# Performance work log

Measured on AMD Instinct MI355X. Metric: run time of the kernel, lower is better.

Reference implementation:

```python
import jax, jax.numpy as jnp
import numpy as np

N_EDGES = 1048576
N_CENTERS = 32768
N_SPECIES = 4
L_MAX = 3
N_BASIS = 12
N_MAX = 8
R_CUT = 5.0
NORM = 1.0 / np.sqrt(32.0)  # hypers['normalize'] = avg_num_neighbors = 32
SH_SPLITS = [0, 1, 4, 9, 16]  # cumulative offsets of (2l+1)


def real_sph_harm_lmax3(u):
    # u: [E,3] unit vectors; returns [E,16] real normalized spherical harmonics (sphericart order m=-l..l)
    x, y, z = u[:, 0], u[:, 1], u[:, 2]
    c0 = 0.5 * np.sqrt(1.0 / np.pi)
    c1 = np.sqrt(3.0 / (4.0 * np.pi))
    x2, y2, z2 = x * x, y * y, z * z
    sh = [
        jnp.full_like(x, c0),
        c1 * y, c1 * z, c1 * x,
        0.5 * np.sqrt(15.0 / np.pi) * x * y,
        0.5 * np.sqrt(15.0 / np.pi) * y * z,
        0.25 * np.sqrt(5.0 / np.pi) * (3.0 * z2 - 1.0),
        0.5 * np.sqrt(15.0 / np.pi) * x * z,
        0.25 * np.sqrt(15.0 / np.pi) * (x2 - y2),
        0.25 * np.sqrt(35.0 / (2.0 * np.pi)) * y * (3.0 * x2 - y2),
        0.5 * np.sqrt(105.0 / np.pi) * x * y * z,
        0.25 * np.sqrt(21.0 / (2.0 * np.pi)) * y * (5.0 * z2 - 1.0),
        0.25 * np.sqrt(7.0 / np.pi) * (5.0 * z2 * z - 3.0 * z),
        0.25 * np.sqrt(21.0 / (2.0 * np.pi)) * x * (5.0 * z2 - 1.0),
        0.25 * np.sqrt(105.0 / np.pi) * z * (x2 - y2),
        0.25 * np.sqrt(35.0 / (2.0 * np.pi)) * x * (x2 - y2),
    ]
    return jnp.stack(sh, axis=1)


def setup_inputs() -> dict:
    key = jax.random.key(0)
    k1, k2, k3, k4 = jax.random.split(key, 4)
    vectors = jax.random.normal(k1, (N_EDGES, 3), dtype=jnp.float32) * 1.5
    radial_weights = jax.random.normal(k2, (L_MAX + 1, N_BASIS, N_MAX), dtype=jnp.float32) * 0.1
    center_index = jax.random.randint(k3, (N_EDGES,), 0, N_CENTERS, dtype=jnp.int64)
    neighbor_species_index = jax.random.randint(k4, (N_EDGES,), 0, N_SPECIES, dtype=jnp.int64)
    return {"vectors": vectors, "radial_weights": radial_weights,
            "center_index": center_index, "neighbor_species_index": neighbor_species_index}


def reference(vectors, radial_weights, center_index, neighbor_species_index):
    # distances and unit vectors
    r = jnp.sqrt(jnp.sum(vectors * vectors, axis=-1) + 1e-12)  # [E]
    u = vectors / r[:, None]
    # smooth radial basis phi_n(r) = sin((n+1) pi r / r_cut)/r, normalized (LE-like)
    ns = jnp.arange(1, N_BASIS + 1, dtype=vectors.dtype)
    phi = jnp.sin(np.pi / R_CUT * r[:, None] * ns[None, :]) / r[:, None] * NORM  # [E, N_BASIS]
    sh = real_sph_harm_lmax3(u)  # [E,16]
    # scatter target: (center, neighbor_species) channel
    idx = center_index * N_SPECIES + neighbor_species_index  # [E]
    densities = []
    for l in range(L_MAX + 1):
        m_l = 2 * l + 1
        sh_l = jax.lax.slice_in_dim(sh, SH_SPLITS[l], SH_SPLITS[l + 1], axis=1)  # [E, 2l+1]
        rad_l = phi @ radial_weights[l]  # [E, N_MAX]
        edge_l = rad_l[:, None, :] * sh_l[:, :, None]  # [E, 2l+1, N_MAX] outer product
        dens = jax.ops.segment_sum(edge_l.reshape(edge_l.shape[0], -1), idx,
                                   num_segments=N_CENTERS * N_SPECIES)  # [N*S, m*n]
        dens = dens.reshape(N_CENTERS, N_SPECIES, m_l, N_MAX)
        dens = jnp.transpose(dens, (0, 2, 1, 3)).reshape(N_CENTERS, m_l, N_SPECIES * N_MAX)
        densities.append(dens)  # c^{a_i l}_{Ai, m, a_j n}
    # concatenate the per-l TensorMap blocks along the m axis -> [N, sum(2l+1), S*N_MAX]
    return jnp.concatenate(densities, axis=1)
```

## Files before the change

kernel.cpp:

```cpp
#include <hip/hip_runtime.h>
#include <math.h>

#define N_EDGES     1048576
#define NBKT        4096
#define SEG_PER_BKT 32
#define N_BASIS     12
#define CAP         384
#define HBLK        64
#define HEPB        (N_EDGES / HBLK)

#define WS_BLKHIST  0
#define WS_TOTALS   (HBLK * NBKT * 2)
#define WS_OFFSETS  (WS_TOTALS + NBKT * 4)
#define WS_REC      (WS_OFFSETS + NBKT * 4)
#define WS_NEED     (WS_REC + (size_t)N_EDGES * 16)

__device__ __forceinline__ void compute_edge(float x, float y, float z,
                                             float* __restrict__ ph,
                                             float* __restrict__ sh)
{
    const float r2    = fmaf(x, x, fmaf(y, y, z * z)) + 1e-12f;
    const float inv_r = rsqrtf(r2);
    const float r     = r2 * inv_r;
    x *= inv_r; y *= inv_r; z *= inv_r;

    const float t = 0.6283185307179586f * r;
    float s1, c1;
    __sincosf(t, &s1, &c1);
    const float twoc = 2.0f * c1;
    const float scale = 0.17677669529663687f * inv_r;
    float skm1 = 0.0f, sk = s1;
    #pragma unroll
    for (int b = 0; b < N_BASIS; ++b) {
        ph[b] = sk * scale;
        const float nxt = fmaf(twoc, sk, -skm1);
        skm1 = sk; sk = nxt;
    }

    const float x2 = x * x, y2 = y * y, z2 = z * z;
    sh[0]  = 0.28209479177387814f;
    sh[1]  = 0.4886025119029199f * y;
    sh[2]  = 0.4886025119029199f * z;
    sh[3]  = 0.4886025119029199f * x;
    sh[4]  = 1.0925484305920792f * x * y;
    sh[5]  = 1.0925484305920792f * y * z;
    sh[6]  = 0.31539156525252005f * (3.0f * z2 - 1.0f);
    sh[7]  = 1.0925484305920792f * x * z;
    sh[8]  = 0.5462742152960396f * (x2 - y2);
    sh[9]  = 0.5900435899266435f * y * (3.0f * x2 - y2);
    sh[10] = 2.890611442640554f  * x * y * z;
    sh[11] = 0.4570457994644658f * y * (5.0f * z2 - 1.0f);
    sh[12] = 0.3731763325901154f * (5.0f * z2 * z - 3.0f * z);
    sh[13] = 0.4570457994644658f * x * (5.0f * z2 - 1.0f);
    sh[14] = 1.445305721320277f  * z * (x2 - y2);
    sh[15] = 0.5900435899266435f * x * (x2 - y2);
}

__global__ __launch_bounds__(1024) void hist_kernel(
    const int* __restrict__ cidx, const int* __restrict__ sidx,
    unsigned short* __restrict__ blkhist)
{
    __shared__ int h[NBKT];
    const int t = threadIdx.x;
    #pragma unroll
    for (int i = t; i < NBKT; i += 1024) h[i] = 0;
    __syncthreads();
    const int base = blockIdx.x * HEPB;
    #pragma unroll
    for (int k = 0; k < HEPB / 1024; ++k) {
        const int e = base + k * 1024 + t;
        const int seg = (cidx[e] << 2) | sidx[e];
        atomicAdd(&h[seg >> 5], 1);
    }
    __syncthreads();
    #pragma unroll
    for (int i = t; i < NBKT; i += 1024)
        blkhist[blockIdx.x * NBKT + i] = (unsigned short)h[i];
}

__global__ __launch_bounds__(1024) void partition16_kernel(
    const int* __restrict__ cidx, const int* __restrict__ sidx,
    const float* __restrict__ vectors,
    const unsigned short* __restrict__ blkhist,
    float4* __restrict__ rec16,
    int* __restrict__ offsets_g, int* __restrict__ totals_g)
{
    __shared__ int ps[1024];
    __shared__ int bb[NBKT];
    __shared__ int lcnt[NBKT];
    const int t  = threadIdx.x;
    const int me = blockIdx.x;

    int tot0 = 0, tot1 = 0, tot2 = 0, tot3 = 0;
    int bef0 = 0, bef1 = 0, bef2 = 0, bef3 = 0;
    for (int blk = 0; blk < HBLK; ++blk) {
        const ushort4 hv = ((const ushort4*)(blkhist + blk * NBKT))[t];
        tot0 += hv.x; tot1 += hv.y; tot2 += hv.z; tot3 += hv.w;
        if (blk < me) { bef0 += hv.x; bef1 += hv.y; bef2 += hv.z; bef3 += hv.w; }
    }
    const int quad = tot0 + tot1 + tot2 + tot3;
    ps[t] = quad;
    __syncthreads();
    #pragma unroll
    for (int d = 1; d < 1024; d <<= 1) {
        const int v = (t >= d) ? ps[t - d] : 0;
        __syncthreads();
        ps[t] += v;
        __syncthreads();
    }
    const int ex = ps[t] - quad;
    const int e0 = ex, e1 = ex + tot0, e2 = e1 + tot1, e3 = e2 + tot2;
    bb[4 * t + 0] = e0 + bef0;
    bb[4 * t + 1] = e1 + bef1;
    bb[4 * t + 2] = e2 + bef2;
    bb[4 * t + 3] = e3 + bef3;
    lcnt[4 * t + 0] = 0; lcnt[4 * t + 1] = 0;
    lcnt[4 * t + 2] = 0; lcnt[4 * t + 3] = 0;
    if (me == 0) {
        offsets_g[4 * t + 0] = e0;  totals_g[4 * t + 0] = tot0;
        offsets_g[4 * t + 1] = e1;  totals_g[4 * t + 1] = tot1;
        offsets_g[4 * t + 2] = e2;  totals_g[4 * t + 2] = tot2;
        offsets_g[4 * t + 3] = e3;  totals_g[4 * t + 3] = tot3;
    }
    __syncthreads();

    const int base = me * HEPB;
    #pragma unroll
    for (int k = 0; k < HEPB / 1024; ++k) {
        const int e = base + k * 1024 + t;
        const int seg = (cidx[e] << 2) | sidx[e];
        const int bkt = seg >> 5;
        const float x = vectors[3 * e + 0];
        const float y = vectors[3 * e + 1];
        const float z = vectors[3 * e + 2];
        const int r = atomicAdd(&lcnt[bkt], 1);
        rec16[bb[bkt] + r] = make_float4(x, y, z, __int_as_float(seg & 31));
    }
}

__global__ __launch_bounds__(256) void compute16_kernel(
    const float4* __restrict__ rec16,
    const int* __restrict__ offsets, const int* __restrict__ counts,
    const float* __restrict__ rw,
    float* __restrict__ out)
{
    __shared__ float4 pay[CAP * 7];
    __shared__ int shist[SEG_PER_BKT];
    __shared__ int soff[SEG_PER_BKT + 1];
    __shared__ int scur[SEG_PER_BKT];

    const int t = threadIdx.x;
    const int b = blockIdx.x;
    const int n = t & 7;
    const int g = t >> 3;

    const int off = offsets[b];
    const int cnt = counts[b];

    if (cnt > CAP) {
        float Wn[4][N_BASIS];
        #pragma unroll
        for (int l = 0; l < 4; ++l)
            #pragma unroll
            for (int bb2 = 0; bb2 < N_BASIS; ++bb2)
                Wn[l][bb2] = rw[(l * N_BASIS + bb2) * 8 + n];
        float acc[16];
        #pragma unroll
        for (int L = 0; L < 16; ++L) acc[L] = 0.0f;
        for (int j = 0; j < cnt; ++j) {
            const float4 v = rec16[off + j];
            if (__float_as_int(v.w) != g) continue;
            float ph[N_BASIS], sh[16];
            compute_edge(v.x, v.y, v.z, ph, sh);
            float rad[4];
            #pragma unroll
            for (int l = 0; l < 4; ++l) {
                float a = 0.0f;
                #pragma unroll
                for (int bb2 = 0; bb2 < N_BASIS; ++bb2)
                    a = fmaf(ph[bb2], Wn[l][bb2], a);
                rad[l] = a;
            }
            #pragma unroll
            for (int L = 0; L < 16; ++L) {
                const int l = (L == 0) ? 0 : (L < 4) ? 1 : (L < 9) ? 2 : 3;
                acc[L] = fmaf(sh[L], rad[l], acc[L]);
            }
        }
        const int seg = b * SEG_PER_BKT + g;
        float* op = out + (size_t)(seg >> 2) * 512 + (seg & 3) * 8 + n;
        #pragma unroll
        for (int L = 0; L < 16; ++L) op[L * 32] = acc[L];
        return;
    }

    if (t < SEG_PER_BKT) shist[t] = 0;
    __syncthreads();

    float4 recs[2];
    const int iters = (cnt + 255) >> 8;
    #pragma unroll
    for (int it = 0; it < 2; ++it) {
        const int i = it * 256 + t;
        if (it < iters && i < cnt) {
            recs[it] = rec16[off + i];
            atomicAdd(&shist[__float_as_int(recs[it].w)], 1);
        }
    }
    __syncthreads();

    if (t < SEG_PER_BKT) {
        const int h = shist[t];
        int v = h;
        #pragma unroll
        for (int d = 1; d < 32; d <<= 1) {
            const int u = __shfl_up(v, d, 32);
            if (t >= d) v += u;
        }
        soff[t] = v - h;
        scur[t] = v - h;
        if (t == 31) soff[32] = v;
    }
    __syncthreads();

    #pragma unroll
    for (int it = 0; it < 2; ++it) {
        const int i = it * 256 + t;
        if (it < iters && i < cnt) {
            const int sl = __float_as_int(recs[it].w);
            const int r = atomicAdd(&scur[sl], 1);
            float ph[N_BASIS], sh[16];
            compute_edge(recs[it].x, recs[it].y, recs[it].z, ph, sh);
            float4* pp = &pay[r * 7];
            pp[0] = make_float4(ph[0], ph[1], ph[2], ph[3]);
            pp[1] = make_float4(ph[4], ph[5], ph[6], ph[7]);
            pp[2] = make_float4(ph[8], ph[9], ph[10], ph[11]);
            pp[3] = make_float4(sh[0], sh[1], sh[2], sh[3]);
            pp[4] = make_float4(sh[4], sh[5], sh[6], sh[7]);
            pp[5] = make_float4(sh[8], sh[9], sh[10], sh[11]);
            pp[6] = make_float4(sh[12], sh[13], sh[14], sh[15]);
        }
    }
    __syncthreads();

    float Wn[4][N_BASIS];
    #pragma unroll
    for (int l = 0; l < 4; ++l)
        #pragma unroll
        for (int bb2 = 0; bb2 < N_BASIS; ++bb2)
            Wn[l][bb2] = rw[(l * N_BASIS + bb2) * 8 + n];

    const int js = soff[g];
    const int je = soff[g + 1];

    float acc[16];
    #pragma unroll
    for (int L = 0; L < 16; ++L) acc[L] = 0.0f;

    for (int j = js; j < je; ++j) {
        const float4* pp = &pay[j * 7];
        const float4 p0 = pp[0], p1 = pp[1], p2 = pp[2];
        const float4 s0 = pp[3], s1 = pp[4], s2 = pp[5], s3 = pp[6];

        float rad[4];
        #pragma unroll
        for (int l = 0; l < 4; ++l) {
            float a =      p0.x * Wn[l][0];
            a = fmaf(p0.y, Wn[l][1],  a);
            a = fmaf(p0.z, Wn[l][2],  a);
            a = fmaf(p0.w, Wn[l][3],  a);
            a = fmaf(p1.x, Wn[l][4],  a);
            a = fmaf(p1.y, Wn[l][5],  a);
            a = fmaf(p1.z, Wn[l][6],  a);
            a = fmaf(p1.w, Wn[l][7],  a);
            a = fmaf(p2.x, Wn[l][8],  a);
            a = fmaf(p2.y, Wn[l][9],  a);
            a = fmaf(p2.z, Wn[l][10], a);
            a = fmaf(p2.w, Wn[l][11], a);
            rad[l] = a;
        }
        acc[0]  = fmaf(s0.x, rad[0], acc[0]);
        acc[1]  = fmaf(s0.y, rad[1], acc[1]);
        acc[2]  = fmaf(s0.z, rad[1], acc[2]);
        acc[3]  = fmaf(s0.w, rad[1], acc[3]);
        acc[4]  = fmaf(s1.x, rad[2], acc[4]);
        acc[5]  = fmaf(s1.y, rad[2], acc[5]);
        acc[6]  = fmaf(s1.z, rad[2], acc[6]);
        acc[7]  = fmaf(s1.w, rad[2], acc[7]);
        acc[8]  = fmaf(s2.x, rad[2], acc[8]);
        acc[9]  = fmaf(s2.y, rad[3], acc[9]);
        acc[10] = fmaf(s2.z, rad[3], acc[10]);
        acc[11] = fmaf(s2.w, rad[3], acc[11]);
        acc[12] = fmaf(s3.x, rad[3], acc[12]);
        acc[13] = fmaf(s3.y, rad[3], acc[13]);
        acc[14] = fmaf(s3.z, rad[3], acc[14]);
        acc[15] = fmaf(s3.w, rad[3], acc[15]);
    }

    const int seg = b * SEG_PER_BKT + g;
    float* op = out + (size_t)(seg >> 2) * 512 + (seg & 3) * 8 + n;
    #pragma unroll
    for (int L = 0; L < 16; ++L) op[L * 32] = acc[L];
}

__global__ __launch_bounds__(256) void atomic_kernel(
    const float* __restrict__ vectors, const float* __restrict__ rw,
    const int* __restrict__ cidx, const int* __restrict__ sidx,
    float* __restrict__ out)
{
    const int e = blockIdx.x * 256 + threadIdx.x;
    if (e >= N_EDGES) return;
    float ph[N_BASIS], sh[16];
    compute_edge(vectors[3*e], vectors[3*e+1], vectors[3*e+2], ph, sh);
    float* op = out + (size_t)cidx[e] * 512 + sidx[e] * 8;
    for (int l = 0; l < 4; ++l) {
        const int L0 = l * l;
        const int ml = 2 * l + 1;
        for (int nn = 0; nn < 8; ++nn) {
            float rad = 0.0f;
            for (int bb2 = 0; bb2 < N_BASIS; ++bb2)
                rad = fmaf(ph[bb2], rw[(l * N_BASIS + bb2) * 8 + nn], rad);
            for (int mm = 0; mm < ml; ++mm)
                atomicAdd(op + (L0 + mm) * 32 + nn, sh[L0 + mm] * rad);
        }
    }
}

extern "C" void kernel_launch(void* const* d_in, const int* in_sizes, int n_in,
                              void* d_out, int out_size, void* d_ws, size_t ws_size,
                              hipStream_t stream) {
    const float* vectors = (const float*)d_in[0];
    const float* rw      = (const float*)d_in[1];
    const int*   cidx    = (const int*)d_in[2];
    const int*   sidx    = (const int*)d_in[3];
    float*       out     = (float*)d_out;

    if (ws_size < (size_t)WS_NEED) {
        hipMemsetAsync(out, 0, (size_t)out_size * sizeof(float), stream);
        hipLaunchKernelGGL(atomic_kernel, dim3(N_EDGES / 256), dim3(256), 0, stream,
                           vectors, rw, cidx, sidx, out);
        return;
    }

    char* ws = (char*)d_ws;
    unsigned short* blkhist = (unsigned short*)(ws + WS_BLKHIST);
    int*            totals  = (int*)(ws + WS_TOTALS);
    int*            offsets = (int*)(ws + WS_OFFSETS);
    float4*         rec16   = (float4*)(ws + WS_REC);

    hipLaunchKernelGGL(hist_kernel,        dim3(HBLK), dim3(1024), 0, stream, cidx, sidx, blkhist);
    hipLaunchKernelGGL(partition16_kernel, dim3(HBLK), dim3(1024), 0, stream, cidx, sidx, vectors, blkhist, rec16, offsets, totals);
    hipLaunchKernelGGL(compute16_kernel,   dim3(NBKT), dim3(256),  0, stream, rec16, offsets, totals, rw, out);
}
```

Before: 179.5 us.

## Partition compact edge indices instead of float4 records and split scan into kernels

The partition pass now writes a 4-byte record (slot<<20 | edge id) instead of a 16-byte float4 holding the vector, and the compute kernel gathers the vectors by edge id. The per-block histogram scan moves out of the partition kernel into two separate scan kernels, and the histogram and partition grids grow from 64 to 256 blocks of 256 threads. This cuts scatter write traffic and redundant per-block prefix work, and exposes more parallelism in the early stages. The cost is two extra launches, a serial single-block scan, and random gathers of vectors in the compute stage.

```diff
diff --git a/kernel.cpp b/kernel.cpp
--- a/kernel.cpp
+++ b/kernel.cpp
@@ -6,14 +6,15 @@
 #define SEG_PER_BKT 32
 #define N_BASIS     12
 #define CAP         384
-#define HBLK        64
+#define HBLK        256
 #define HEPB        (N_EDGES / HBLK)
 
+
 #define WS_BLKHIST  0
-#define WS_TOTALS   (HBLK * NBKT * 2)
+#define WS_TOTALS   (HBLK * NBKT * 4)
 #define WS_OFFSETS  (WS_TOTALS + NBKT * 4)
 #define WS_REC      (WS_OFFSETS + NBKT * 4)
-#define WS_NEED     (WS_REC + (size_t)N_EDGES * 16)
+#define WS_NEED     (WS_REC + (size_t)N_EDGES * 4)
 
 __device__ __forceinline__ void compute_edge(float x, float y, float z,
                                              float* __restrict__ ph,
@@ -56,91 +57,93 @@
     sh[15] = 0.5900435899266435f * x * (x2 - y2);
 }
 
-__global__ __launch_bounds__(1024) void hist_kernel(
+__global__ __launch_bounds__(256) void hist_kernel(
     const int* __restrict__ cidx, const int* __restrict__ sidx,
-    unsigned short* __restrict__ blkhist)
+    int* __restrict__ blkhist)
 {
     __shared__ int h[NBKT];
     const int t = threadIdx.x;
     #pragma unroll
-    for (int i = t; i < NBKT; i += 1024) h[i] = 0;
+    for (int i = t; i < NBKT; i += 256) h[i] = 0;
     __syncthreads();
     const int base = blockIdx.x * HEPB;
     #pragma unroll
-    for (int k = 0; k < HEPB / 1024; ++k) {
-        const int e = base + k * 1024 + t;
+    for (int k = 0; k < HEPB / 256; ++k) {
+        const int e = base + k * 256 + t;
         const int seg = (cidx[e] << 2) | sidx[e];
         atomicAdd(&h[seg >> 5], 1);
     }
     __syncthreads();
     #pragma unroll
-    for (int i = t; i < NBKT; i += 1024)
-        blkhist[blockIdx.x * NBKT + i] = (unsigned short)h[i];
-}
-
-__global__ __launch_bounds__(1024) void partition16_kernel(
+    for (int i = t; i < NBKT; i += 256)
+        blkhist[blockIdx.x * NBKT + i] = h[i];
+}
+
+__global__ __launch_bounds__(128) void scanA_kernel(
+    int* __restrict__ blkhist, int* __restrict__ totals)
+{
+    const int bkt = blockIdx.x * 128 + threadIdx.x;
+    int run = 0;
+    for (int blk = 0; blk < HBLK; ++blk) {
+        const int v = blkhist[blk * NBKT + bkt];
+        blkhist[blk * NBKT + bkt] = run;
+        run += v;
+    }
+    totals[bkt] = run;
+}
+
+__global__ __launch_bounds__(1024) void scanB_kernel(
+    const int* __restrict__ totals, int* __restrict__ offsets)
+{
+    __shared__ int tmp[1024];
+    const int t = threadIdx.x;
+    const int4 tv = ((const int4*)totals)[t];
+    const int a0 = tv.x, a1 = a0 + tv.y, a2 = a1 + tv.z, a3 = a2 + tv.w;
+    tmp[t] = a3;
+    __syncthreads();
+    #pragma unroll
+    for (int d = 1; d < 1024; d <<= 1) {
+        const int v = (t >= d) ? tmp[t - d] : 0;
+        __syncthreads();
+        tmp[t] += v;
+        __syncthreads();
+    }
+    const int ex = tmp[t] - a3;
+    offsets[4 * t + 0] = ex;
+    offsets[4 * t + 1] = ex + a0;
+    offsets[4 * t + 2] = ex + a1;
+    offsets[4 * t + 3] = ex + a2;
+}
+
+__global__ __launch_bounds__(256) void partition_kernel(
     const int* __restrict__ cidx, const int* __restrict__ sidx,
-    const float* __restrict__ vectors,
-    const unsigned short* __restrict__ blkhist,
-    float4* __restrict__ rec16,
-    int* __restrict__ offsets_g, int* __restrict__ totals_g)
-{
-    __shared__ int ps[1024];
+    const int* __restrict__ blkhist, const int* __restrict__ offsets,
+    unsigned int* __restrict__ records)
+{
     __shared__ int bb[NBKT];
     __shared__ int lcnt[NBKT];
-    const int t  = threadIdx.x;
-    const int me = blockIdx.x;
-
-    int tot0 = 0, tot1 = 0, tot2 = 0, tot3 = 0;
-    int bef0 = 0, bef1 = 0, bef2 = 0, bef3 = 0;
-    for (int blk = 0; blk < HBLK; ++blk) {
-        const ushort4 hv = ((const ushort4*)(blkhist + blk * NBKT))[t];
-        tot0 += hv.x; tot1 += hv.y; tot2 += hv.z; tot3 += hv.w;
-        if (blk < me) { bef0 += hv.x; bef1 += hv.y; bef2 += hv.z; bef3 += hv.w; }
-    }
-    const int quad = tot0 + tot1 + tot2 + tot3;
-    ps[t] = quad;
-    __syncthreads();
-    #pragma unroll
-    for (int d = 1; d < 1024; d <<= 1) {
-        const int v = (t >= d) ? ps[t - d] : 0;
-        __syncthreads();
-        ps[t] += v;
-        __syncthreads();
-    }
-    const int ex = ps[t] - quad;
-    const int e0 = ex, e1 = ex + tot0, e2 = e1 + tot1, e3 = e2 + tot2;
-    bb[4 * t + 0] = e0 + bef0;
-    bb[4 * t + 1] = e1 + bef1;
-    bb[4 * t + 2] = e2 + bef2;
-    bb[4 * t + 3] = e3 + bef3;
-    lcnt[4 * t + 0] = 0; lcnt[4 * t + 1] = 0;
-    lcnt[4 * t + 2] = 0; lcnt[4 * t + 3] = 0;
-    if (me == 0) {
-        offsets_g[4 * t + 0] = e0;  totals_g[4 * t + 0] = tot0;
-        offsets_g[4 * t + 1] = e1;  totals_g[4 * t + 1] = tot1;
-        offsets_g[4 * t + 2] = e2;  totals_g[4 * t + 2] = tot2;
-        offsets_g[4 * t + 3] = e3;  totals_g[4 * t + 3] = tot3;
-    }
-    __syncthreads();
-
-    const int base = me * HEPB;
-    #pragma unroll
-    for (int k = 0; k < HEPB / 1024; ++k) {
-        const int e = base + k * 1024 + t;
+    const int t = threadIdx.x;
+    #pragma unroll
+    for (int i = t; i < NBKT; i += 256) {
+        bb[i] = offsets[i] + blkhist[blockIdx.x * NBKT + i];
+        lcnt[i] = 0;
+    }
+    __syncthreads();
+    const int base = blockIdx.x * HEPB;
+    #pragma unroll
+    for (int k = 0; k < HEPB / 256; ++k) {
+        const int e = base + k * 256 + t;
         const int seg = (cidx[e] << 2) | sidx[e];
         const int bkt = seg >> 5;
-        const float x = vectors[3 * e + 0];
-        const float y = vectors[3 * e + 1];
-        const float z = vectors[3 * e + 2];
         const int r = atomicAdd(&lcnt[bkt], 1);
-        rec16[bb[bkt] + r] = make_float4(x, y, z, __int_as_float(seg & 31));
-    }
-}
-
-__global__ __launch_bounds__(256) void compute16_kernel(
-    const float4* __restrict__ rec16,
+        records[bb[bkt] + r] = ((unsigned)(seg & 31) << 20) | (unsigned)e;
+    }
+}
+
+__global__ __launch_bounds__(256) void compute_kernel(
+    const unsigned int* __restrict__ records,
     const int* __restrict__ offsets, const int* __restrict__ counts,
+    const float* __restrict__ vectors,
     const float* __restrict__ rw,
     float* __restrict__ out)
 {
@@ -168,10 +171,11 @@
         #pragma unroll
         for (int L = 0; L < 16; ++L) acc[L] = 0.0f;
         for (int j = 0; j < cnt; ++j) {
-            const float4 v = rec16[off + j];
-            if (__float_as_int(v.w) != g) continue;
+            const unsigned rec = records[off + j];
+            if ((int)(rec >> 20) != g) continue;
+            const int eid = rec & 0xFFFFF;
             float ph[N_BASIS], sh[16];
-            compute_edge(v.x, v.y, v.z, ph, sh);
+            compute_edge(vectors[3*eid], vectors[3*eid+1], vectors[3*eid+2], ph, sh);
             float rad[4];
             #pragma unroll
             for (int l = 0; l < 4; ++l) {
@@ -197,14 +201,14 @@
     if (t < SEG_PER_BKT) shist[t] = 0;
     __syncthreads();
 
-    float4 recs[2];
+    unsigned recs[2];
     const int iters = (cnt + 255) >> 8;
     #pragma unroll
     for (int it = 0; it < 2; ++it) {
         const int i = it * 256 + t;
         if (it < iters && i < cnt) {
-            recs[it] = rec16[off + i];
-            atomicAdd(&shist[__float_as_int(recs[it].w)], 1);
+            recs[it] = records[off + i];
+            atomicAdd(&shist[recs[it] >> 20], 1);
         }
     }
     __syncthreads();
@@ -227,10 +231,14 @@
     for (int it = 0; it < 2; ++it) {
         const int i = it * 256 + t;
         if (it < iters && i < cnt) {
-            const int sl = __float_as_int(recs[it].w);
+            const int sl  = recs[it] >> 20;
+            const int eid = recs[it] & 0xFFFFF;
+            const float x = vectors[3 * eid + 0];
+            const float y = vectors[3 * eid + 1];
+            const float z = vectors[3 * eid + 2];
             const int r = atomicAdd(&scur[sl], 1);
             float ph[N_BASIS], sh[16];
-            compute_edge(recs[it].x, recs[it].y, recs[it].z, ph, sh);
+            compute_edge(x, y, z, ph, sh);
             float4* pp = &pay[r * 7];
             pp[0] = make_float4(ph[0], ph[1], ph[2], ph[3]);
             pp[1] = make_float4(ph[4], ph[5], ph[6], ph[7]);
@@ -343,12 +351,14 @@
     }
 
     char* ws = (char*)d_ws;
-    unsigned short* blkhist = (unsigned short*)(ws + WS_BLKHIST);
-    int*            totals  = (int*)(ws + WS_TOTALS);
-    int*            offsets = (int*)(ws + WS_OFFSETS);
-    float4*         rec16   = (float4*)(ws + WS_REC);
-
-    hipLaunchKernelGGL(hist_kernel,        dim3(HBLK), dim3(1024), 0, stream, cidx, sidx, blkhist);
-    hipLaunchKernelGGL(partition16_kernel, dim3(HBLK), dim3(1024), 0, stream, cidx, sidx, vectors, blkhist, rec16, offsets, totals);
-    hipLaunchKernelGGL(compute16_kernel,   dim3(NBKT), dim3(256),  0, stream, rec16, offsets, totals, rw, out);
-}
+    int*          blkhist = (int*)(ws + WS_BLKHIST);
+    int*          totals  = (int*)(ws + WS_TOTALS);
+    int*          offsets = (int*)(ws + WS_OFFSETS);
+    unsigned int* records = (unsigned int*)(ws + WS_REC);
+
+    hipLaunchKernelGGL(hist_kernel,      dim3(HBLK),     dim3(256),  0, stream, cidx, sidx, blkhist);
+    hipLaunchKernelGGL(scanA_kernel,     dim3(NBKT/128), dim3(128),  0, stream, blkhist, totals);
+    hipLaunchKernelGGL(scanB_kernel,     dim3(1),        dim3(1024), 0, stream, totals, offsets);
+    hipLaunchKernelGGL(partition_kernel, dim3(HBLK),     dim3(256),  0, stream, cidx, sidx, blkhist, offsets, records);
+    hipLaunchKernelGGL(compute_kernel,   dim3(NBKT),     dim3(256),  0, stream, records, offsets, totals, vectors, rw, out);
+}
```

New measurement: 153.6 us. 14.4% less time.
